# Performance work log

Hardware: AMD Instinct MI355X
Metric: run time of the kernel (lower is better)

Reference implementation:

```python
import jax, jax.numpy as jnp
import numpy as np

EPS = 1e-5

def setup_inputs() -> dict:
    key = jax.random.key(0)
    ks = jax.random.split(key, 4)
    B, C, A, T = 32, 1536, 128, 1000  # batch, in_channels, attention_channels, time
    x = jax.random.normal(ks[0], (B, C, T), dtype=jnp.float32)
    # attention MLP: Conv1d(3C -> A, k=1) -> ReLU -> BN(A) -> Conv1d(A -> C, k=1)
    w1 = jax.random.normal(ks[1], (A, 3 * C), dtype=jnp.float32) / np.float32(np.sqrt(3 * C))
    b1 = jnp.zeros((A,), jnp.float32)
    g1 = jnp.ones((A,), jnp.float32)
    be1 = jnp.zeros((A,), jnp.float32)
    rm1 = jnp.zeros((A,), jnp.float32)
    rv1 = jnp.ones((A,), jnp.float32)
    w2 = jax.random.normal(ks[2], (C, A), dtype=jnp.float32) / np.float32(np.sqrt(A))
    b2 = jnp.zeros((C,), jnp.float32)
    # final BatchNorm1d over 2C pooled features
    g2 = jnp.ones((2 * C,), jnp.float32)
    be2 = jnp.zeros((2 * C,), jnp.float32)
    rm2 = jnp.zeros((2 * C,), jnp.float32)
    rv2 = jnp.ones((2 * C,), jnp.float32)
    return {"x": x, "w1": w1, "b1": b1, "g1": g1, "be1": be1, "rm1": rm1, "rv1": rv1,
            "w2": w2, "b2": b2, "g2": g2, "be2": be2, "rm2": rm2, "rv2": rv2}

def reference(x, w1, b1, g1, be1, rm1, rv1, w2, b2, g2, be2, rm2, rv2):
    # x: [B, C, T]
    mean_x = jnp.mean(x, axis=2, keepdims=True)                       # [B,C,1]
    std_x = jnp.sqrt(jnp.var(x, axis=2, ddof=1, keepdims=True) + EPS)  # unbiased var
    cat = jnp.concatenate([x,
                           jnp.broadcast_to(mean_x, x.shape),
                           jnp.broadcast_to(std_x, x.shape)], axis=1)  # [B,3C,T]
    # conv1x1 == channel matmul
    h = jnp.einsum('ac,bct->bat', w1, cat) + b1[None, :, None]         # [B,A,T]
    h = jax.nn.relu(h)
    # BatchNorm1d(A), inference mode with running stats
    h = (h - rm1[None, :, None]) * (g1 / jnp.sqrt(rv1 + EPS))[None, :, None] + be1[None, :, None]
    logits = jnp.einsum('ca,bat->bct', w2, h) + b2[None, :, None]      # [B,C,T]
    attn = jax.nn.softmax(logits, axis=2)
    xs = x * attn
    mu = jnp.sum(xs, axis=2)                                           # [B,C]
    sum_sq = jnp.sum(xs * x, axis=2)                                   # [B,C]
    sigma = jnp.sqrt(jnp.abs(sum_sq - mu ** 2) + EPS)
    pool = jnp.concatenate([mu, sigma], axis=1)                        # [B,2C]
    # final BatchNorm1d(2C), inference mode
    return (pool - rm2) * (g2 / jnp.sqrt(rv2 + EPS)) + be2
```

## Files before the change

kernel.cpp:

```cpp
#include <hip/hip_runtime.h>
#include <hip/hip_bf16.h>

#define BATCH 32
#define CCH   1536
#define ACH   128
#define TLEN  1000
#define TPAD  1024
#define TSPLIT 4
#define TCHUNK 256
#define EPSV  1e-5f
#define NINF  -3.0e38f
#define LOG2E 1.4426950408889634f
#define RTHR  11.5f

typedef __attribute__((ext_vector_type(8))) short bf16x8;
typedef __attribute__((ext_vector_type(4))) float f32x4;

__device__ __forceinline__ unsigned short f2bf(float f) {
    union { float f; unsigned u; } v; v.f = f;
    unsigned r = v.u + 0x7fffu + ((v.u >> 16) & 1u);
    return (unsigned short)(r >> 16);
}
__device__ __forceinline__ float bf2f(unsigned short u) {
    union { unsigned u; float f; } v; v.u = ((unsigned)u) << 16;
    return v.f;
}

__global__ __launch_bounds__(256) void kA(const float* __restrict__ x,
                                          unsigned short* __restrict__ xt,
                                          float* __restrict__ meanw,
                                          float* __restrict__ stdw) {
    int b = blockIdx.y, cb = blockIdx.x * 32;
    int tid = threadIdx.x;
    int row = tid >> 3, l8 = tid & 7;
    __shared__ float tile[64][33];
    const float* xr = x + ((size_t)(b * CCH + cb + row)) * TLEN;
    float s1 = 0.f, s2 = 0.f;
    for (int tt = 0; tt < 16; ++tt) {
        int t0 = tt * 64;
        #pragma unroll
        for (int p = 0; p < 2; ++p) {
            int tf = t0 + (l8 + 8 * p) * 4;
            float4 vv = make_float4(0.f, 0.f, 0.f, 0.f);
            if (tf < TLEN) vv = *reinterpret_cast<const float4*>(xr + tf);
            s1 += vv.x + vv.y + vv.z + vv.w;
            s2 += vv.x * vv.x + vv.y * vv.y + vv.z * vv.z + vv.w * vv.w;
            int tl = tf - t0;
            tile[tl + 0][row] = vv.x;
            tile[tl + 1][row] = vv.y;
            tile[tl + 2][row] = vv.z;
            tile[tl + 3][row] = vv.w;
        }
        __syncthreads();
        int tl = tid >> 2, c8 = (tid & 3) * 8;
        unsigned o[4];
        #pragma unroll
        for (int j = 0; j < 4; ++j) {
            unsigned lo = f2bf(tile[tl][c8 + 2 * j]);
            unsigned hi = f2bf(tile[tl][c8 + 2 * j + 1]);
            o[j] = lo | (hi << 16);
        }
        uint4 u; u.x = o[0]; u.y = o[1]; u.z = o[2]; u.w = o[3];
        *reinterpret_cast<uint4*>(xt + ((size_t)(b * TPAD + t0 + tl)) * CCH + cb + c8) = u;
        __syncthreads();
    }
    #pragma unroll
    for (int d = 1; d < 8; d <<= 1) { s1 += __shfl_xor(s1, d); s2 += __shfl_xor(s2, d); }
    if (l8 == 0) {
        float mean = s1 / (float)TLEN;
        float var = (s2 - s1 * s1 / (float)TLEN) / (float)(TLEN - 1);
        meanw[b * CCH + cb + row] = mean;
        stdw[b * CCH + cb + row] = sqrtf(var + EPSV);
    }
}

__global__ __launch_bounds__(256) void kA2(const float* __restrict__ x,
                                           float* __restrict__ meanw,
                                           float* __restrict__ stdw) {
    int b = blockIdx.y, cb = blockIdx.x * 32;
    int tid = threadIdx.x;
    int row = tid >> 3, l8 = tid & 7;
    const float* xr = x + ((size_t)(b * CCH + cb + row)) * TLEN;
    float s1 = 0.f, s2 = 0.f;
    for (int tf = l8 * 4; tf < TLEN; tf += 32) {
        float4 vv = *reinterpret_cast<const float4*>(xr + tf);
        s1 += vv.x + vv.y + vv.z + vv.w;
        s2 += vv.x * vv.x + vv.y * vv.y + vv.z * vv.z + vv.w * vv.w;
    }
    #pragma unroll
    for (int d = 1; d < 8; d <<= 1) { s1 += __shfl_xor(s1, d); s2 += __shfl_xor(s2, d); }
    if (l8 == 0) {
        float mean = s1 / (float)TLEN;
        float var = (s2 - s1 * s1 / (float)TLEN) / (float)(TLEN - 1);
        meanw[b * CCH + cb + row] = mean;
        stdw[b * CCH + cb + row] = sqrtf(var + EPSV);
    }
}

__global__ __launch_bounds__(256) void kB1(const float* __restrict__ w1,
                                           unsigned short* __restrict__ w1x) {
    int e = blockIdx.x * 256 + threadIdx.x;
    int a = e / CCH, c = e - a * CCH;
    w1x[e] = f2bf(w1[(size_t)a * (3 * CCH) + c]);
}

__global__ __launch_bounds__(64) void kB2(const float* __restrict__ w1,
                                          const float* __restrict__ b1,
                                          const float* __restrict__ meanw,
                                          const float* __restrict__ stdw,
                                          float* __restrict__ hbias) {
    int a = blockIdx.x, b = blockIdx.y, l = threadIdx.x;
    const float* wr = w1 + (size_t)a * 3 * CCH;
    const float* mb = meanw + b * CCH;
    const float* sb = stdw + b * CCH;
    float acc = 0.f;
    for (int k = l; k < CCH; k += 64)
        acc += wr[CCH + k] * mb[k] + wr[2 * CCH + k] * sb[k];
    #pragma unroll
    for (int d = 1; d < 64; d <<= 1) acc += __shfl_xor(acc, d);
    if (l == 0) hbias[b * ACH + a] = acc + b1[a];
}

__global__ __launch_bounds__(64) void kB3(const float* __restrict__ w2,
                                          const float* __restrict__ b2,
                                          const float* __restrict__ g1,
                                          const float* __restrict__ be1,
                                          const float* __restrict__ rm1,
                                          const float* __restrict__ rv1,
                                          unsigned short* __restrict__ w2e,
                                          float* __restrict__ b2e) {
    int c = blockIdx.x, l = threadIdx.x;
    float acc = 0.f;
    #pragma unroll
    for (int p = 0; p < 2; ++p) {
        int a = p * 64 + l;
        float s1 = g1[a] / sqrtf(rv1[a] + EPSV);
        float w = w2[(size_t)c * ACH + a];
        w2e[(size_t)c * ACH + a] = f2bf(w * s1 * LOG2E);
        acc += w * (be1[a] - s1 * rm1[a]);
    }
    #pragma unroll
    for (int d = 1; d < 64; d <<= 1) acc += __shfl_xor(acc, d);
    if (l == 0) b2e[c] = (b2[c] + acc) * LOG2E;
}

__global__ __launch_bounds__(512) void kC3(const unsigned short* __restrict__ xt,
                                           const unsigned short* __restrict__ w1x,
                                           const float* __restrict__ hbias,
                                           unsigned short* __restrict__ h) {
    int b = blockIdx.y;
    int t0 = blockIdx.x * 64;
    int tid = threadIdx.x;
    int wv = tid >> 6, l = tid & 63, g = l >> 4, r = l & 15;
    int a0 = (wv & 3) * 32;
    int tw = (wv >> 2) * 32;

    __shared__ uint4 As[2][1024];
    __shared__ uint4 Bs[2][512];

    const unsigned short* bG = xt + (size_t)(b * TPAD + t0) * CCH;

    int qa0 = tid, qa1 = tid + 512, qb = tid;
    int wa0 = qa0 ^ ((qa0 >> 3) & 7), wa1 = qa1 ^ ((qa1 >> 3) & 7), wb = qb ^ ((qb >> 3) & 7);
    int arow0 = qa0 >> 3, arow1 = qa1 >> 3, acol = (qa0 & 7) * 8;
    int brow = qb >> 3, bcol = (qb & 7) * 8;

    As[0][wa0] = *reinterpret_cast<const uint4*>(w1x + (size_t)arow0 * CCH + acol);
    As[0][wa1] = *reinterpret_cast<const uint4*>(w1x + (size_t)arow1 * CCH + acol);
    Bs[0][wb]  = *reinterpret_cast<const uint4*>(bG + (size_t)brow * CCH + bcol);
    __syncthreads();

    f32x4 acc[2][2];
    #pragma unroll
    for (int i = 0; i < 2; ++i)
        #pragma unroll
        for (int j = 0; j < 2; ++j) acc[i][j] = f32x4{0.f, 0.f, 0.f, 0.f};

    for (int ks = 0; ks < CCH / 64; ++ks) {
        int buf = ks & 1;
        uint4 na0, na1, nb;
        if (ks < CCH / 64 - 1) {
            int cofs = (ks + 1) * 64;
            na0 = *reinterpret_cast<const uint4*>(w1x + (size_t)arow0 * CCH + cofs + acol);
            na1 = *reinterpret_cast<const uint4*>(w1x + (size_t)arow1 * CCH + cofs + acol);
            nb  = *reinterpret_cast<const uint4*>(bG + (size_t)brow * CCH + cofs + bcol);
        }
        bf16x8 Af[2][2], Bf[2][2];
        #pragma unroll
        for (int at = 0; at < 2; ++at) {
            int row = a0 + 16 * at + r;
            #pragma unroll
            for (int kk = 0; kk < 2; ++kk) {
                int ch = (row * 8 + kk * 4 + g) ^ (row & 7);
                Af[at][kk] = *reinterpret_cast<const bf16x8*>(&As[buf][ch]);
            }
        }
        #pragma unroll
        for (int tt = 0; tt < 2; ++tt) {
            int row = tw + 16 * tt + r;
            #pragma unroll
            for (int kk = 0; kk < 2; ++kk) {
                int ch = (row * 8 + kk * 4 + g) ^ (row & 7);
                Bf[tt][kk] = *reinterpret_cast<const bf16x8*>(&Bs[buf][ch]);
            }
        }
        #pragma unroll
        for (int kk = 0; kk < 2; ++kk)
            #pragma unroll
            for (int at = 0; at < 2; ++at)
                #pragma unroll
                for (int tt = 0; tt < 2; ++tt)
                    acc[at][tt] = __builtin_amdgcn_mfma_f32_16x16x32_bf16(Af[at][kk], Bf[tt][kk], acc[at][tt], 0, 0, 0);
        if (ks < CCH / 64 - 1) {
            As[buf ^ 1][wa0] = na0;
            As[buf ^ 1][wa1] = na1;
            Bs[buf ^ 1][wb]  = nb;
        }
        __syncthreads();
    }

    #pragma unroll
    for (int at = 0; at < 2; ++at) {
        f32x4 hb = *reinterpret_cast<const f32x4*>(hbias + b * ACH + a0 + 16 * at + 4 * g);
        #pragma unroll
        for (int tt = 0; tt < 2; ++tt) {
            int t = t0 + tw + 16 * tt + r;
            float v0 = acc[at][tt][0] + hb[0]; v0 = v0 > 0.f ? v0 : 0.f;
            float v1 = acc[at][tt][1] + hb[1]; v1 = v1 > 0.f ? v1 : 0.f;
            float v2 = acc[at][tt][2] + hb[2]; v2 = v2 > 0.f ? v2 : 0.f;
            float v3 = acc[at][tt][3] + hb[3]; v3 = v3 > 0.f ? v3 : 0.f;
            uint2 u;
            u.x = (unsigned)f2bf(v0) | ((unsigned)f2bf(v1) << 16);
            u.y = (unsigned)f2bf(v2) | ((unsigned)f2bf(v3) << 16);
            *reinterpret_cast<uint2*>(h + ((size_t)(b * TPAD + t)) * ACH + a0 + 16 * at + 4 * g) = u;
        }
    }
}

__global__ __launch_bounds__(256) void kC2(const float* __restrict__ x,
                                           const unsigned short* __restrict__ w1x,
                                           const float* __restrict__ hbias,
                                           unsigned short* __restrict__ h) {
    int b = blockIdx.y;
    int t0 = blockIdx.x * 32;
    int tid = threadIdx.x;
    int wv = tid >> 6, l = tid & 63, g = l >> 4, r = l & 15;
    const unsigned short* aptr = w1x + (size_t)(32 * wv + r) * CCH + 8 * g;
    f32x4 acc[2][2];
    #pragma unroll
    for (int i = 0; i < 2; ++i)
        #pragma unroll
        for (int j = 0; j < 2; ++j) acc[i][j] = f32x4{0.f, 0.f, 0.f, 0.f};
    for (int kk = 0; kk < CCH / 32; ++kk) {
        bf16x8 Af[2], Bf[2];
        #pragma unroll
        for (int at = 0; at < 2; ++at)
            Af[at] = *reinterpret_cast<const bf16x8*>(aptr + (size_t)(16 * at) * CCH + 32 * kk);
        #pragma unroll
        for (int tt = 0; tt < 2; ++tt) {
            int t = t0 + 16 * tt + r;
            unsigned short tmp[8];
            #pragma unroll
            for (int j = 0; j < 8; ++j) {
                float xv = 0.f;
                if (t < TLEN) xv = x[((size_t)(b * CCH + 32 * kk + 8 * g + j)) * TLEN + t];
                tmp[j] = f2bf(xv);
            }
            Bf[tt] = *reinterpret_cast<const bf16x8*>(tmp);
        }
        #pragma unroll
        for (int at = 0; at < 2; ++at)
            #pragma unroll
            for (int tt = 0; tt < 2; ++tt)
                acc[at][tt] = __builtin_amdgcn_mfma_f32_16x16x32_bf16(Af[at], Bf[tt], acc[at][tt], 0, 0, 0);
    }
    #pragma unroll
    for (int at = 0; at < 2; ++at) {
        f32x4 hb = *reinterpret_cast<const f32x4*>(hbias + b * ACH + 32 * wv + 16 * at + 4 * g);
        #pragma unroll
        for (int tt = 0; tt < 2; ++tt) {
            int t = t0 + 16 * tt + r;
            float v0 = acc[at][tt][0] + hb[0]; v0 = v0 > 0.f ? v0 : 0.f;
            float v1 = acc[at][tt][1] + hb[1]; v1 = v1 > 0.f ? v1 : 0.f;
            float v2 = acc[at][tt][2] + hb[2]; v2 = v2 > 0.f ? v2 : 0.f;
            float v3 = acc[at][tt][3] + hb[3]; v3 = v3 > 0.f ? v3 : 0.f;
            uint2 u;
            u.x = (unsigned)f2bf(v0) | ((unsigned)f2bf(v1) << 16);
            u.y = (unsigned)f2bf(v2) | ((unsigned)f2bf(v3) << 16);
            *reinterpret_cast<uint2*>(h + ((size_t)(b * TPAD + t)) * ACH + 32 * wv + 16 * at + 4 * g) = u;
        }
    }
}

__global__ __launch_bounds__(256) void kD3(const unsigned short* __restrict__ xt,
                                           const unsigned short* __restrict__ h,
                                           const unsigned short* __restrict__ w2e,
                                           const float* __restrict__ b2e,
                                           float4* __restrict__ part) {
    int b = blockIdx.y, ts = blockIdx.z;
    int cblk = blockIdx.x * 128;
    int tid = threadIdx.x;
    int wv = tid >> 6, l = tid & 63, g = l >> 4, r = l & 15;
    int c0 = cblk + 32 * wv;
    int t0 = ts * TCHUNK;

    __shared__ uint4 hs[2][512];

    bf16x8 W[2][4];
    f32x4 b2v[2];
    #pragma unroll
    for (int af = 0; af < 2; ++af) {
        #pragma unroll
        for (int kk = 0; kk < 4; ++kk)
            W[af][kk] = *reinterpret_cast<const bf16x8*>(w2e + (size_t)(c0 + 16 * af + r) * ACH + 32 * kk + 8 * g);
        b2v[af] = *reinterpret_cast<const f32x4*>(b2e + c0 + 16 * af + 4 * g);
    }

    const unsigned short* hbase = h + (size_t)(b * TPAD + t0) * ACH;
    const unsigned short* xb = xt + (size_t)(b * TPAD) * CCH;

    int q0 = tid, q1 = tid + 256;
    int w0 = q0 ^ ((q0 >> 4) & 7), w1 = q1 ^ ((q1 >> 4) & 7);

    hs[0][w0] = *reinterpret_cast<const uint4*>(hbase + q0 * 8);
    hs[0][w1] = *reinterpret_cast<const uint4*>(hbase + q1 * 8);
    __syncthreads();

    float m[2][4], s[2][4], wx[2][4], wxx[2][4];
    #pragma unroll
    for (int af = 0; af < 2; ++af)
        #pragma unroll
        for (int i = 0; i < 4; ++i) { m[af][i] = NINF; s[af][i] = 0.f; wx[af][i] = 0.f; wxx[af][i] = 0.f; }

    for (int tc = 0; tc < TCHUNK / 32; ++tc) {
        int buf = tc & 1;
        uint4 n0, n1;
        if (tc < TCHUNK / 32 - 1) {
            const unsigned short* src = hbase + (size_t)(tc + 1) * 32 * ACH;
            n0 = *reinterpret_cast<const uint4*>(src + q0 * 8);
            n1 = *reinterpret_cast<const uint4*>(src + q1 * 8);
        }
        int tb0 = t0 + tc * 32 + r, tb1 = tb0 + 16;
        uint2 xu[2][2];
        #pragma unroll
        for (int af = 0; af < 2; ++af) {
            xu[af][0] = *reinterpret_cast<const uint2*>(xb + (size_t)tb0 * CCH + c0 + 16 * af + 4 * g);
            xu[af][1] = *reinterpret_cast<const uint2*>(xb + (size_t)tb1 * CCH + c0 + 16 * af + 4 * g);
        }

        f32x4 a2[2][2];
        a2[0][0] = f32x4{0.f, 0.f, 0.f, 0.f}; a2[0][1] = f32x4{0.f, 0.f, 0.f, 0.f};
        a2[1][0] = f32x4{0.f, 0.f, 0.f, 0.f}; a2[1][1] = f32x4{0.f, 0.f, 0.f, 0.f};
        #pragma unroll
        for (int tt = 0; tt < 2; ++tt) {
            int tl = tt * 16 + r;
            #pragma unroll
            for (int kk = 0; kk < 4; ++kk) {
                int ch = (tl * 16 + kk * 4 + g) ^ (tl & 7);
                bf16x8 Bf = *reinterpret_cast<const bf16x8*>(&hs[buf][ch]);
                a2[0][tt] = __builtin_amdgcn_mfma_f32_16x16x32_bf16(W[0][kk], Bf, a2[0][tt], 0, 0, 0);
                a2[1][tt] = __builtin_amdgcn_mfma_f32_16x16x32_bf16(W[1][kk], Bf, a2[1][tt], 0, 0, 0);
            }
        }

        bool val0 = (tb0 < TLEN), val1 = (tb1 < TLEN);
        #pragma unroll
        for (int af = 0; af < 2; ++af) {
            float xv0[4], xv1[4];
            xv0[0] = bf2f((unsigned short)(xu[af][0].x & 0xffff));
            xv0[1] = bf2f((unsigned short)(xu[af][0].x >> 16));
            xv0[2] = bf2f((unsigned short)(xu[af][0].y & 0xffff));
            xv0[3] = bf2f((unsigned short)(xu[af][0].y >> 16));
            xv1[0] = bf2f((unsigned short)(xu[af][1].x & 0xffff));
            xv1[1] = bf2f((unsigned short)(xu[af][1].x >> 16));
            xv1[2] = bf2f((unsigned short)(xu[af][1].y & 0xffff));
            xv1[3] = bf2f((unsigned short)(xu[af][1].y >> 16));
            #pragma unroll
            for (int i = 0; i < 4; ++i) {
                float v0 = val0 ? (a2[af][0][i] + b2v[af][i]) : NINF;
                float v1 = val1 ? (a2[af][1][i] + b2v[af][i]) : NINF;
                float mx = fmaxf(v0, v1);
                if (__any(mx > m[af][i] + RTHR)) {
                    float mn = fmaxf(m[af][i], mx);
                    float sc = exp2f(m[af][i] - mn);
                    s[af][i] *= sc; wx[af][i] *= sc; wxx[af][i] *= sc; m[af][i] = mn;
                }
                float e0 = exp2f(v0 - m[af][i]);
                float e1 = exp2f(v1 - m[af][i]);
                float xe0 = xv0[i] * e0, xe1 = xv1[i] * e1;
                s[af][i]   += e0 + e1;
                wx[af][i]  += xe0 + xe1;
                wxx[af][i] += xv0[i] * xe0 + xv1[i] * xe1;
            }
        }

        if (tc < TCHUNK / 32 - 1) {
            hs[buf ^ 1][w0] = n0;
            hs[buf ^ 1][w1] = n1;
        }
        __syncthreads();
    }

    #pragma unroll
    for (int af = 0; af < 2; ++af)
        #pragma unroll
        for (int i = 0; i < 4; ++i) {
            float mm = m[af][i], ss = s[af][i], sx = wx[af][i], sxx = wxx[af][i];
            #pragma unroll
            for (int d = 1; d < 16; d <<= 1) {
                float mo = __shfl_xor(mm, d);
                float so = __shfl_xor(ss, d);
                float xo = __shfl_xor(sx, d);
                float qo = __shfl_xor(sxx, d);
                float mn = fmaxf(mm, mo);
                float fa = exp2f(mm - mn), fb = exp2f(mo - mn);
                ss = ss * fa + so * fb;
                sx = sx * fa + xo * fb;
                sxx = sxx * fa + qo * fb;
                mm = mn;
            }
            if (r == 0) {
                int c = c0 + 16 * af + 4 * g + i;
                float4 p; p.x = mm; p.y = ss; p.z = sx; p.w = sxx;
                part[((size_t)(b * TSPLIT + ts)) * CCH + c] = p;
            }
        }
}

__global__ __launch_bounds__(256) void kD1(const float* __restrict__ x,
                                           const unsigned short* __restrict__ h,
                                           const unsigned short* __restrict__ w2e,
                                           const float* __restrict__ b2e,
                                           float4* __restrict__ part) {
    int b = blockIdx.y, ts = blockIdx.z;
    int cblk = blockIdx.x * 64;
    int tid = threadIdx.x;
    int wv = tid >> 6, l = tid & 63, g = l >> 4, r = l & 15;
    int c0 = cblk + 16 * wv;
    int t0 = ts * TCHUNK;
    __shared__ float xs[2][64][36];

    bf16x8 W[4];
    #pragma unroll
    for (int kk = 0; kk < 4; ++kk)
        W[kk] = *reinterpret_cast<const bf16x8*>(w2e + (size_t)(c0 + r) * ACH + 32 * kk + 8 * g);
    f32x4 b2v = *reinterpret_cast<const f32x4*>(b2e + c0 + 4 * g);

    int sc_ = tid >> 2;
    int st_ = (tid & 3) * 8;
    const float* xrow = x + ((size_t)(b * CCH + cblk + sc_)) * TLEN;
    const unsigned short* hb = h + (size_t)(b * TPAD) * ACH + 8 * g;

    auto stage = [&](int buf, int tc) {
        int tg = t0 + tc * 32;
        #pragma unroll
        for (int p = 0; p < 2; ++p) {
            int tl = st_ + 4 * p;
            float4 v = make_float4(0.f, 0.f, 0.f, 0.f);
            if (tg + tl < TLEN) v = *reinterpret_cast<const float4*>(xrow + tg + tl);
            *reinterpret_cast<float4*>(&xs[buf][sc_][tl]) = v;
        }
    };

    float m[4], s[4], wx[4], wxx[4];
    #pragma unroll
    for (int i = 0; i < 4; ++i) { m[i] = NINF; s[i] = 0.f; wx[i] = 0.f; wxx[i] = 0.f; }

    stage(0, 0);
    __syncthreads();
    for (int tc = 0; tc < TCHUNK / 32; ++tc) {
        int buf = tc & 1;
        if (tc + 1 < TCHUNK / 32) stage(buf ^ 1, tc + 1);
        f32x4 a2[2];
        a2[0] = f32x4{0.f, 0.f, 0.f, 0.f};
        a2[1] = f32x4{0.f, 0.f, 0.f, 0.f};
        #pragma unroll
        for (int tt = 0; tt < 2; ++tt) {
            int t = t0 + tc * 32 + tt * 16 + r;
            #pragma unroll
            for (int kk = 0; kk < 4; ++kk) {
                bf16x8 Bf = *reinterpret_cast<const bf16x8*>(hb + (size_t)t * ACH + 32 * kk);
                a2[tt] = __builtin_amdgcn_mfma_f32_16x16x32_bf16(W[kk], Bf, a2[tt], 0, 0, 0);
            }
        }
        int tb = t0 + tc * 32 + r;
        bool val0 = (tb < TLEN), val1 = (tb + 16 < TLEN);
        #pragma unroll
        for (int i = 0; i < 4; ++i) {
            int cl = 16 * wv + 4 * g + i;
            float v0 = val0 ? (a2[0][i] + b2v[i]) : NINF;
            float v1 = val1 ? (a2[1][i] + b2v[i]) : NINF;
            float mx = fmaxf(v0, v1);
            if (mx > m[i] + RTHR) {
                float sc = exp2f(m[i] - mx);
                s[i] *= sc; wx[i] *= sc; wxx[i] *= sc; m[i] = mx;
            }
            float e0 = exp2f(v0 - m[i]);
            float e1 = exp2f(v1 - m[i]);
            float x0 = xs[buf][cl][r];
            float x1 = xs[buf][cl][r + 16];
            float xe0 = x0 * e0, xe1 = x1 * e1;
            s[i]   += e0 + e1;
            wx[i]  += xe0 + xe1;
            wxx[i] += x0 * xe0 + x1 * xe1;
        }
        __syncthreads();
    }

    #pragma unroll
    for (int i = 0; i < 4; ++i) {
        float mm = m[i], ss = s[i], sx = wx[i], sxx = wxx[i];
        #pragma unroll
        for (int d = 1; d < 16; d <<= 1) {
            float mo = __shfl_xor(mm, d);
            float so = __shfl_xor(ss, d);
            float xo = __shfl_xor(sx, d);
            float qo = __shfl_xor(sxx, d);
            float mn = fmaxf(mm, mo);
            float fa = exp2f(mm - mn), fb = exp2f(mo - mn);
            ss = ss * fa + so * fb;
            sx = sx * fa + xo * fb;
            sxx = sxx * fa + qo * fb;
            mm = mn;
        }
        if (r == 0) {
            int c = c0 + 4 * g + i;
            float4 p; p.x = mm; p.y = ss; p.z = sx; p.w = sxx;
            part[((size_t)(b * TSPLIT + ts)) * CCH + c] = p;
        }
    }
}

__global__ __launch_bounds__(256) void kE(const float4* __restrict__ part,
                                          const float* __restrict__ rm2,
                                          const float* __restrict__ rv2,
                                          const float* __restrict__ g2,
                                          const float* __restrict__ be2,
                                          float* __restrict__ out) {
    int idx = blockIdx.x * 256 + threadIdx.x;
    int b = idx / CCH, c = idx - b * CCH;
    float m = NINF, s = 0.f, wx = 0.f, wxx = 0.f;
    #pragma unroll
    for (int ts = 0; ts < TSPLIT; ++ts) {
        float4 p = part[((size_t)(b * TSPLIT + ts)) * CCH + c];
        float mn = fmaxf(m, p.x);
        float fa = exp2f(m - mn), fb = exp2f(p.x - mn);
        s = s * fa + p.y * fb;
        wx = wx * fa + p.z * fb;
        wxx = wxx * fa + p.w * fb;
        m = mn;
    }
    float mu = wx / s;
    float ssq = wxx / s;
    float sig = sqrtf(fabsf(ssq - mu * mu) + EPSV);
    out[b * 2 * CCH + c] = (mu - rm2[c]) * g2[c] * rsqrtf(rv2[c] + EPSV) + be2[c];
    int c2 = CCH + c;
    out[b * 2 * CCH + c2] = (sig - rm2[c2]) * g2[c2] * rsqrtf(rv2[c2] + EPSV) + be2[c2];
}

extern "C" void kernel_launch(void* const* d_in, const int* in_sizes, int n_in,
                              void* d_out, int out_size, void* d_ws, size_t ws_size,
                              hipStream_t stream) {
    const float* x   = (const float*)d_in[0];
    const float* w1  = (const float*)d_in[1];
    const float* b1  = (const float*)d_in[2];
    const float* g1  = (const float*)d_in[3];
    const float* be1 = (const float*)d_in[4];
    const float* rm1 = (const float*)d_in[5];
    const float* rv1 = (const float*)d_in[6];
    const float* w2  = (const float*)d_in[7];
    const float* b2  = (const float*)d_in[8];
    const float* g2  = (const float*)d_in[9];
    const float* be2 = (const float*)d_in[10];
    const float* rm2 = (const float*)d_in[11];
    const float* rv2 = (const float*)d_in[12];
    float* out = (float*)d_out;

    const size_t sz_xt    = (size_t)BATCH * TPAD * CCH * 2;
    const size_t sz_h     = (size_t)BATCH * TPAD * ACH * 2;
    const size_t sz_w1x   = (size_t)ACH * CCH * 2;
    const size_t sz_w2e   = (size_t)CCH * ACH * 2;
    const size_t sz_mean  = (size_t)BATCH * CCH * 4;
    const size_t sz_std   = sz_mean;
    const size_t sz_hbias = (size_t)BATCH * ACH * 4;
    const size_t sz_b2e   = (size_t)CCH * 4;
    const size_t sz_part  = (size_t)BATCH * TSPLIT * CCH * 16;
    const size_t need_small = sz_h + sz_w1x + sz_w2e + sz_mean + sz_std + sz_hbias + sz_b2e + sz_part;
    bool use_xt = (ws_size >= need_small + sz_xt);

    char* ws = (char*)d_ws;
    unsigned short* xt = nullptr;
    if (use_xt) { xt = (unsigned short*)ws; ws += sz_xt; }
    unsigned short* hbuf = (unsigned short*)ws; ws += sz_h;
    unsigned short* w1x  = (unsigned short*)ws; ws += sz_w1x;
    unsigned short* w2e  = (unsigned short*)ws; ws += sz_w2e;
    float* meanw = (float*)ws; ws += sz_mean;
    float* stdw  = (float*)ws; ws += sz_std;
    float* hbias = (float*)ws; ws += sz_hbias;
    float* b2e   = (float*)ws; ws += sz_b2e;
    float4* part = (float4*)ws; ws += sz_part;

    if (use_xt)
        kA<<<dim3(48, 32), 256, 0, stream>>>(x, xt, meanw, stdw);
    else
        kA2<<<dim3(48, 32), 256, 0, stream>>>(x, meanw, stdw);
    kB1<<<(ACH * CCH) / 256, 256, 0, stream>>>(w1, w1x);
    kB3<<<CCH, 64, 0, stream>>>(w2, b2, g1, be1, rm1, rv1, w2e, b2e);
    kB2<<<dim3(ACH, BATCH), 64, 0, stream>>>(w1, b1, meanw, stdw, hbias);
    if (use_xt) {
        kC3<<<dim3(TPAD / 64, BATCH), 512, 0, stream>>>(xt, w1x, hbias, hbuf);
        kD3<<<dim3(CCH / 128, BATCH, TSPLIT), 256, 0, stream>>>(xt, hbuf, w2e, b2e, part);
    } else {
        kC2<<<dim3(TPAD / 32, BATCH), 256, 0, stream>>>(x, w1x, hbias, hbuf);
        kD1<<<dim3(CCH / 64, BATCH, TSPLIT), 256, 0, stream>>>(x, hbuf, w2e, b2e, part);
    }
    kE<<<(BATCH * CCH) / 256, 256, 0, stream>>>(part, rm2, rv2, g2, be2, out);
}
```

Baseline: 170.3 us.

## Double-buffer transpose tile in kA and widen block to 64 channels

Restructures the transpose/stats kernel to use a two-slot shared-memory tile with register prefetch, so global loads for the next 64-step slice are issued while the current slice is converted to bf16 and stored. This also removes one barrier per iteration. The block now covers 64 channels with 512 threads, producing 128-byte bf16 row segments per store instead of 64-byte. The cost is more shared memory per block and fewer blocks in flight, which may reduce occupancy.

```diff
diff --git a/kernel.cpp b/kernel.cpp
--- a/kernel.cpp
+++ b/kernel.cpp
@@ -26,44 +26,66 @@
     return v.f;
 }
 
-__global__ __launch_bounds__(256) void kA(const float* __restrict__ x,
+__global__ __launch_bounds__(512) void kA(const float* __restrict__ x,
                                           unsigned short* __restrict__ xt,
                                           float* __restrict__ meanw,
                                           float* __restrict__ stdw) {
-    int b = blockIdx.y, cb = blockIdx.x * 32;
+    int b = blockIdx.y, cb = blockIdx.x * 64;
     int tid = threadIdx.x;
     int row = tid >> 3, l8 = tid & 7;
-    __shared__ float tile[64][33];
+    __shared__ float tile[2][64][65];
     const float* xr = x + ((size_t)(b * CCH + cb + row)) * TLEN;
+
     float s1 = 0.f, s2 = 0.f;
-    for (int tt = 0; tt < 16; ++tt) {
-        int t0 = tt * 64;
+    float4 rA[2];
+
+    auto loadTile = [&](int it) {
         #pragma unroll
         for (int p = 0; p < 2; ++p) {
-            int tf = t0 + (l8 + 8 * p) * 4;
+            int tf = it * 64 + p * 32 + l8 * 4;
             float4 vv = make_float4(0.f, 0.f, 0.f, 0.f);
             if (tf < TLEN) vv = *reinterpret_cast<const float4*>(xr + tf);
+            rA[p] = vv;
             s1 += vv.x + vv.y + vv.z + vv.w;
             s2 += vv.x * vv.x + vv.y * vv.y + vv.z * vv.z + vv.w * vv.w;
-            int tl = tf - t0;
-            tile[tl + 0][row] = vv.x;
-            tile[tl + 1][row] = vv.y;
-            tile[tl + 2][row] = vv.z;
-            tile[tl + 3][row] = vv.w;
-        }
+        }
+    };
+    auto writeTile = [&](int buf) {
+        #pragma unroll
+        for (int p = 0; p < 2; ++p) {
+            int tl = p * 32 + l8 * 4;
+            tile[buf][tl + 0][row] = rA[p].x;
+            tile[buf][tl + 1][row] = rA[p].y;
+            tile[buf][tl + 2][row] = rA[p].z;
+            tile[buf][tl + 3][row] = rA[p].w;
+        }
+    };
+    auto readStore = [&](int buf, int it) {
+        int tl = tid >> 3;
+        int c8 = (tid & 7) * 8;
+        unsigned o[4];
+        #pragma unroll
+        for (int j = 0; j < 4; ++j) {
+            unsigned lo = f2bf(tile[buf][tl][c8 + 2 * j]);
+            unsigned hi = f2bf(tile[buf][tl][c8 + 2 * j + 1]);
+            o[j] = lo | (hi << 16);
+        }
+        uint4 u; u.x = o[0]; u.y = o[1]; u.z = o[2]; u.w = o[3];
+        *reinterpret_cast<uint4*>(xt + ((size_t)(b * TPAD + it * 64 + tl)) * CCH + cb + c8) = u;
+    };
+
+    loadTile(0);
+    writeTile(0);
+    loadTile(1);
+    __syncthreads();
+    for (int it = 0; it < 16; ++it) {
+        int buf = it & 1;
+        if (it < 15) writeTile(buf ^ 1);
+        if (it < 14) loadTile(it + 2);
+        readStore(buf, it);
         __syncthreads();
-        int tl = tid >> 2, c8 = (tid & 3) * 8;
-        unsigned o[4];
-        #pragma unroll
-        for (int j = 0; j < 4; ++j) {
-            unsigned lo = f2bf(tile[tl][c8 + 2 * j]);
-            unsigned hi = f2bf(tile[tl][c8 + 2 * j + 1]);
-            o[j] = lo | (hi << 16);
-        }
-        uint4 u; u.x = o[0]; u.y = o[1]; u.z = o[2]; u.w = o[3];
-        *reinterpret_cast<uint4*>(xt + ((size_t)(b * TPAD + t0 + tl)) * CCH + cb + c8) = u;
-        __syncthreads();
-    }
+    }
+
     #pragma unroll
     for (int d = 1; d < 8; d <<= 1) { s1 += __shfl_xor(s1, d); s2 += __shfl_xor(s2, d); }
     if (l8 == 0) {
@@ -601,7 +623,7 @@
     float4* part = (float4*)ws; ws += sz_part;
 
     if (use_xt)
-        kA<<<dim3(48, 32), 256, 0, stream>>>(x, xt, meanw, stdw);
+        kA<<<dim3(CCH / 64, BATCH), 512, 0, stream>>>(x, xt, meanw, stdw);
     else
         kA2<<<dim3(48, 32), 256, 0, stream>>>(x, meanw, stdw);
     kB1<<<(ACH * CCH) / 256, 256, 0, stream>>>(w1, w1x);
```

Measured after the change: 150.5 us. 11.6% less time.
